# Kernel optimization log

Hardware: AMD Instinct MI355X
Metric: run time of the kernel (lower is better)

Reference implementation:

```python
import jax, jax.numpy as jnp
import numpy as np

B, QL, KL = 8, 2048, 2048
QD, KD, ED = 1024, 1024, 1024


def setup_inputs() -> dict:
    key = jax.random.key(0)
    ks = jax.random.split(key, 11)
    s = 0.02
    return {
        "query": jax.random.normal(ks[0], (B, QL, QD), jnp.float32),
        "key_value": jax.random.normal(ks[1], (B, KL, KD), jnp.float32),
        "mask": jnp.ones((B, QL, KL), jnp.int32),
        "Wq": jax.random.normal(ks[2], (QD, ED), jnp.float32) * s,
        "bq": jnp.zeros((ED,), jnp.float32),
        "Wk": jax.random.normal(ks[3], (KD, ED), jnp.float32) * s,
        "bk": jnp.zeros((ED,), jnp.float32),
        "Wv": jax.random.normal(ks[4], (KD, ED), jnp.float32) * s,
        "bv": jnp.zeros((ED,), jnp.float32),
        "Wo": jax.random.normal(ks[5], (ED, ED), jnp.float32) * s,
        "bo": jnp.zeros((ED,), jnp.float32),
    }


def reference(query, key_value, mask, Wq, bq, Wk, bk, Wv, bv, Wo, bo):
    # Linear projections
    Q = jnp.einsum('bqd,de->bqe', query, Wq) + bq      # (B, QL, E)
    K = jnp.einsum('bkd,de->bke', key_value, Wk) + bk  # (B, KL, E)
    V = jnp.einsum('bkd,de->bke', key_value, Wv) + bv  # (B, KL, E)
    scale = 1.0 / jnp.sqrt(jnp.asarray(Q.shape[-1], Q.dtype))
    scores = jnp.einsum('bqe,bke->bqk', Q, K) * scale  # (B, QL, KL)
    scores = jnp.where(mask == 0, -jnp.inf, scores)
    attn = jax.nn.softmax(scores, axis=-1)             # (B, QL, KL)
    # dropout is identity in eval mode
    attended = jnp.einsum('bqk,bke->bqe', attn, V)     # (B, QL, E)
    out = jnp.einsum('bqe,ef->bqf', attended, Wo) + bo
    return out, attn
```

## Files before the change

kernel.cpp:

```cpp
#include <hip/hip_runtime.h>
#include <hip/hip_bf16.h>
#include <math.h>


typedef __attribute__((ext_vector_type(8))) short short8;
typedef __attribute__((ext_vector_type(4))) float floatx4;

__device__ __forceinline__ unsigned short f2bf(float x) {
  return __builtin_bit_cast(unsigned short, __float2bfloat16(x));
}
__device__ __forceinline__ float bf2f(unsigned short s) {
  unsigned int u = ((unsigned int)s) << 16;
  return __builtin_bit_cast(float, u);
}

typedef const unsigned int __attribute__((address_space(1))) ga_u32;
typedef unsigned int __attribute__((address_space(3))) lds_u32;
__device__ __forceinline__ void gl_lds16(const void* g, void* l) {
  __builtin_amdgcn_global_load_lds((ga_u32*)g, (lds_u32*)l, 16, 0, 0);
}

template <int EPI>
__global__ __launch_bounds__(512, 2) void gemm8(
    const unsigned short* __restrict__ Ah,
    const unsigned short* __restrict__ Bh, void* __restrict__ Cp,
    unsigned short* __restrict__ Cl, const float* __restrict__ bias,
    float alpha, int M, int N, int K, int Mt, long long sA, long long sB,
    long long sC) {
  extern __shared__ char smem[];

  const int gx = gridDim.x;
  const int gxy = gx * gridDim.y;
  const int nwg = gxy * gridDim.z;
  const int orig = blockIdx.z * gxy + blockIdx.y * gx + blockIdx.x;
  const int wg = (orig & 7) * (nwg >> 3) + (orig >> 3);
  const int zb_i = wg / gxy;
  const int rem = wg - zb_i * gxy;
  const int by = rem / gx;
  const int bx = rem - by * gx;
  const int m0 = by * 256, n0 = bx * 256;
  const long long zb = zb_i;

  const unsigned short* Ag = Ah + zb * sA;
  const unsigned short* Bg = Bh + zb * sB;

  const int t = threadIdx.x;
  const int srow = t >> 3;
  const int skw = ((t & 7) << 3) ^ ((srow & 7) << 3);
  const unsigned short* aS = Ag + (long long)(m0 + srow) * K + skw;
  const unsigned short* bS = Bg + (long long)(n0 + srow) * K + skw;
  char* dstA = smem + t * 16;
  char* dstB = smem + 65536 + t * 16;

  const int lane = t & 63;
  const int wv = t >> 6, wy = wv >> 2, wx = wv & 3;
  const int lm = lane & 15, q = lane >> 4;
  const int x0 = (q << 4) ^ ((lm & 7) << 4);
  const int aB0 = (wy * 128 + lm) * 128;
  const int bB0 = 65536 + (wx * 64 + lm) * 128;
  const int aRd0 = aB0 + x0, aRd1 = aB0 + (x0 ^ 64);
  const int bRd0 = bB0 + x0, bRd1 = bB0 + (x0 ^ 64);

  floatx4 acc[8][4];
#pragma unroll
  for (int i = 0; i < 8; ++i)
#pragma unroll
    for (int j = 0; j < 4; ++j) acc[i][j] = (floatx4)(0.0f);

  short8 fa[4][2];
  short8 fb[2][2][2];

#pragma unroll
  for (int c = 0; c < 4; ++c) {
    gl_lds16(aS + (long long)(c * 64) * K, dstA + c * 8192);
    gl_lds16(bS + (long long)(c * 64) * K, dstB + c * 8192);
  }
  gl_lds16(aS + 64, dstA + 32768);
  gl_lds16(bS + 64, dstB + 32768);
  gl_lds16(aS + 64LL * K + 64, dstA + 32768 + 8192);
  gl_lds16(bS + 64LL * K + 64, dstB + 32768 + 8192);
  asm volatile("s_waitcnt vmcnt(4)" ::: "memory");
  __builtin_amdgcn_s_barrier();

  auto tile = [&](int kt, int bo, int nbo) {
    const bool p1 = (kt + 64) < K;
    const bool p2 = (kt + 128) < K;
#pragma unroll
    for (int mt = 0; mt < 4; ++mt) {
      fa[mt][0] = *(const short8*)(smem + (bo + aRd0 + mt * 2048));
      fa[mt][1] = *(const short8*)(smem + (bo + aRd1 + mt * 2048));
    }
#pragma unroll
    for (int nt = 0; nt < 2; ++nt) {
      fb[0][nt][0] = *(const short8*)(smem + (bo + bRd0 + nt * 2048));
      fb[0][nt][1] = *(const short8*)(smem + (bo + bRd1 + nt * 2048));
    }
    if (p1) {
      gl_lds16(aS + 128LL * K + (kt + 64), dstA + nbo + 16384);
      gl_lds16(bS + 128LL * K + (kt + 64), dstB + nbo + 16384);
    }
    __builtin_amdgcn_s_barrier();
    __builtin_amdgcn_s_setprio(1);
#pragma unroll
    for (int mt = 0; mt < 4; ++mt)
#pragma unroll
      for (int nt = 0; nt < 2; ++nt) {
        acc[mt][nt] = __builtin_amdgcn_mfma_f32_16x16x32_bf16(
            fa[mt][0], fb[0][nt][0], acc[mt][nt], 0, 0, 0);
        acc[mt][nt] = __builtin_amdgcn_mfma_f32_16x16x32_bf16(
            fa[mt][1], fb[0][nt][1], acc[mt][nt], 0, 0, 0);
      }
    __builtin_amdgcn_s_setprio(0);
    __builtin_amdgcn_s_barrier();
#pragma unroll
    for (int nt = 0; nt < 2; ++nt) {
      fb[1][nt][0] = *(const short8*)(smem + (bo + bRd0 + 4096 + nt * 2048));
      fb[1][nt][1] = *(const short8*)(smem + (bo + bRd1 + 4096 + nt * 2048));
    }
    if (p1) {
      gl_lds16(aS + 192LL * K + (kt + 64), dstA + nbo + 24576);
      gl_lds16(bS + 192LL * K + (kt + 64), dstB + nbo + 24576);
    }
    __builtin_amdgcn_s_barrier();
    __builtin_amdgcn_s_setprio(1);
#pragma unroll
    for (int mt = 0; mt < 4; ++mt)
#pragma unroll
      for (int nt = 0; nt < 2; ++nt) {
        acc[mt][2 + nt] = __builtin_amdgcn_mfma_f32_16x16x32_bf16(
            fa[mt][0], fb[1][nt][0], acc[mt][2 + nt], 0, 0, 0);
        acc[mt][2 + nt] = __builtin_amdgcn_mfma_f32_16x16x32_bf16(
            fa[mt][1], fb[1][nt][1], acc[mt][2 + nt], 0, 0, 0);
      }
    __builtin_amdgcn_s_setprio(0);
    __builtin_amdgcn_s_barrier();
#pragma unroll
    for (int mt = 0; mt < 4; ++mt) {
      fa[mt][0] = *(const short8*)(smem + (bo + aRd0 + 8192 + mt * 2048));
      fa[mt][1] = *(const short8*)(smem + (bo + aRd1 + 8192 + mt * 2048));
    }
    if (p2) {
      gl_lds16(aS + (kt + 128), dstA + bo);
      gl_lds16(bS + (kt + 128), dstB + bo);
    }
    __builtin_amdgcn_s_barrier();
    __builtin_amdgcn_s_setprio(1);
#pragma unroll
    for (int mt = 0; mt < 4; ++mt)
#pragma unroll
      for (int nt = 0; nt < 2; ++nt) {
        acc[4 + mt][nt] = __builtin_amdgcn_mfma_f32_16x16x32_bf16(
            fa[mt][0], fb[0][nt][0], acc[4 + mt][nt], 0, 0, 0);
        acc[4 + mt][nt] = __builtin_amdgcn_mfma_f32_16x16x32_bf16(
            fa[mt][1], fb[0][nt][1], acc[4 + mt][nt], 0, 0, 0);
      }
    __builtin_amdgcn_s_setprio(0);
    __builtin_amdgcn_s_barrier();
    if (p2) {
      gl_lds16(aS + 64LL * K + (kt + 128), dstA + bo + 8192);
      gl_lds16(bS + 64LL * K + (kt + 128), dstB + bo + 8192);
    }
    __builtin_amdgcn_s_barrier();
    __builtin_amdgcn_s_setprio(1);
#pragma unroll
    for (int mt = 0; mt < 4; ++mt)
#pragma unroll
      for (int nt = 0; nt < 2; ++nt) {
        acc[4 + mt][2 + nt] = __builtin_amdgcn_mfma_f32_16x16x32_bf16(
            fa[mt][0], fb[1][nt][0], acc[4 + mt][2 + nt], 0, 0, 0);
        acc[4 + mt][2 + nt] = __builtin_amdgcn_mfma_f32_16x16x32_bf16(
            fa[mt][1], fb[1][nt][1], acc[4 + mt][2 + nt], 0, 0, 0);
      }
    __builtin_amdgcn_s_setprio(0);
    if (p2) {
      asm volatile("s_waitcnt vmcnt(4)" ::: "memory");
    } else {
      asm volatile("s_waitcnt vmcnt(0)" ::: "memory");
    }
    __builtin_amdgcn_s_barrier();
  };

  for (int kt = 0; kt < K; kt += 128) {
    tile(kt, 0, 32768);
    tile(kt + 64, 32768, 0);
  }

#pragma unroll
  for (int ni = 0; ni < 4; ++ni) {
    const int col = n0 + wx * 64 + ni * 16 + lm;
    const float bvv = bias ? bias[col] : 0.0f;
#pragma unroll
    for (int mi = 0; mi < 8; ++mi) {
      const int rbase = m0 + wy * 128 + mi * 16 + q * 4;
      if constexpr (EPI == 3) {
        const int b = rbase / Mt;
        const int kk = rbase - b * Mt;
        unsigned short* dd =
            (unsigned short*)Cp + (long long)b * sC + (long long)col * Mt + kk;
        ushort4 pk;
        pk.x = f2bf(acc[mi][ni][0] * alpha + bvv);
        pk.y = f2bf(acc[mi][ni][1] * alpha + bvv);
        pk.z = f2bf(acc[mi][ni][2] * alpha + bvv);
        pk.w = f2bf(acc[mi][ni][3] * alpha + bvv);
        *reinterpret_cast<ushort4*>(dd) = pk;
      } else {
#pragma unroll
        for (int i = 0; i < 4; ++i) {
          const long long idx = zb * sC + (long long)(rbase + i) * N + col;
          const float x = acc[mi][ni][i] * alpha + bvv;
          if constexpr (EPI == 1) {
            ((unsigned short*)Cp)[idx] = f2bf(x);
          } else {
            const unsigned short h = f2bf(x);
            ((unsigned short*)Cp)[idx] = h;
            Cl[idx] = f2bf(x - bf2f(h));
          }
        }
      }
    }
  }
}

#define BM 128
#define BN 128
#define BK 32

template <int AMODE, bool BSPL, int EPI>
__global__ __launch_bounds__(256) void gemm_nt(
    const void* __restrict__ Apv, const unsigned short* __restrict__ Alp,
    const unsigned short* __restrict__ Bhp,
    const unsigned short* __restrict__ Blp, void* __restrict__ Cp,
    unsigned short* __restrict__ Cl, const float* __restrict__ bias,
    float alpha, int M, int N, int K, int Mt, long long sA, long long sB,
    long long sC) {
  __shared__ unsigned short As_h[BM * BK];
  __shared__ unsigned short Bs_h[BN * BK];
  __shared__ unsigned short As_l[(AMODE == 2) ? BM * BK : 8];
  __shared__ unsigned short Bs_l[BSPL ? BN * BK : 8];

  const int t = threadIdx.x;
  const int lane = t & 63;
  const int wave = t >> 6;
  const int wy = wave >> 1, wx = wave & 1;
  const int lm = lane & 15, q = lane >> 4;
  const int m0 = blockIdx.y * BM, n0 = blockIdx.x * BN;
  const long long zb = blockIdx.z;

  const unsigned short* Ahg = (const unsigned short*)Apv + zb * sA;
  const unsigned short* Alg = (AMODE == 2) ? (Alp + zb * sA) : nullptr;
  const unsigned short* Bhg = Bhp + zb * sB;
  const unsigned short* Blg = BSPL ? (Blp + zb * sB) : nullptr;

  floatx4 acc[4][4];
#pragma unroll
  for (int i = 0; i < 4; ++i)
#pragma unroll
    for (int j = 0; j < 4; ++j) acc[i][j] = (floatx4)(0.0f);

  const int ch_row = lane >> 2;
  const int ch_off = (lane & 3) << 3;

  for (int k0 = 0; k0 < K; k0 += BK) {
    __syncthreads();
#pragma unroll
    for (int j = 0; j < 2; ++j) {
      const int chunk = wave * 2 + j;
      const int row = chunk * 16 + ch_row;
      gl_lds16(Ahg + (long long)(m0 + row) * K + k0 + ch_off,
               &As_h[chunk * 512 + lane * 8]);
      if constexpr (AMODE == 2)
        gl_lds16(Alg + (long long)(m0 + row) * K + k0 + ch_off,
                 &As_l[chunk * 512 + lane * 8]);
    }
#pragma unroll
    for (int j = 0; j < 2; ++j) {
      const int chunk = wave * 2 + j;
      const int row = chunk * 16 + ch_row;
      gl_lds16(Bhg + (long long)(n0 + row) * K + k0 + ch_off,
               &Bs_h[chunk * 512 + lane * 8]);
      if constexpr (BSPL)
        gl_lds16(Blg + (long long)(n0 + row) * K + k0 + ch_off,
                 &Bs_l[chunk * 512 + lane * 8]);
    }
    __syncthreads();

    short8 fa[4], fb[4], fal[4], fbl[4];
#pragma unroll
    for (int mt = 0; mt < 4; ++mt) {
      const int row = wy * 64 + mt * 16 + lm;
      fa[mt] = *reinterpret_cast<const short8*>(&As_h[row * BK + q * 8]);
      if constexpr (AMODE == 2)
        fal[mt] = *reinterpret_cast<const short8*>(&As_l[row * BK + q * 8]);
    }
#pragma unroll
    for (int nt = 0; nt < 4; ++nt) {
      const int row = wx * 64 + nt * 16 + lm;
      fb[nt] = *reinterpret_cast<const short8*>(&Bs_h[row * BK + q * 8]);
      if constexpr (BSPL)
        fbl[nt] = *reinterpret_cast<const short8*>(&Bs_l[row * BK + q * 8]);
    }

#pragma unroll
    for (int mt = 0; mt < 4; ++mt)
#pragma unroll
      for (int nt = 0; nt < 4; ++nt) {
        acc[mt][nt] = __builtin_amdgcn_mfma_f32_16x16x32_bf16(
            fa[mt], fb[nt], acc[mt][nt], 0, 0, 0);
        if constexpr (AMODE == 2 && BSPL) {
          acc[mt][nt] = __builtin_amdgcn_mfma_f32_16x16x32_bf16(
              fa[mt], fbl[nt], acc[mt][nt], 0, 0, 0);
          acc[mt][nt] = __builtin_amdgcn_mfma_f32_16x16x32_bf16(
              fal[mt], fb[nt], acc[mt][nt], 0, 0, 0);
        }
      }
  }

#pragma unroll
  for (int nt = 0; nt < 4; ++nt) {
    const int col = n0 + wx * 64 + nt * 16 + lm;
    const float bv = bias ? bias[col] : 0.0f;
#pragma unroll
    for (int mt = 0; mt < 4; ++mt) {
      const int rbase = m0 + wy * 64 + mt * 16 + q * 4;
#pragma unroll
      for (int i = 0; i < 4; ++i) {
        const long long idx = zb * sC + (long long)(rbase + i) * N + col;
        const float x = acc[mt][nt][i] * alpha + bv;
        if constexpr (EPI == 0) {
          ((float*)Cp)[idx] = x;
        } else {
          ((unsigned short*)Cp)[idx] = f2bf(x);
        }
      }
    }
  }
}

__global__ __launch_bounds__(256) void cvt_bf16(const float* __restrict__ in,
                                                unsigned short* __restrict__ o,
                                                int n8) {
  const int i = blockIdx.x * 256 + threadIdx.x;
  if (i >= n8) return;
  const float4* p = reinterpret_cast<const float4*>(in) + (long long)i * 2;
  const float4 a = p[0], b = p[1];
  short8 h;
  h[0] = (short)f2bf(a.x); h[1] = (short)f2bf(a.y);
  h[2] = (short)f2bf(a.z); h[3] = (short)f2bf(a.w);
  h[4] = (short)f2bf(b.x); h[5] = (short)f2bf(b.y);
  h[6] = (short)f2bf(b.z); h[7] = (short)f2bf(b.w);
  reinterpret_cast<short8*>(o)[i] = h;
}

__global__ __launch_bounds__(256) void prep_w(const float* __restrict__ W,
                                              unsigned short* __restrict__ Th,
                                              unsigned short* __restrict__ Tl,
                                              int R, int C) {
  __shared__ float tile[32][33];
  const int c0 = blockIdx.x * 32, r0 = blockIdx.y * 32;
  const int tx = threadIdx.x & 31, ty = threadIdx.x >> 5;
#pragma unroll
  for (int i = 0; i < 4; ++i)
    tile[ty + i * 8][tx] = W[(long long)(r0 + ty + i * 8) * C + c0 + tx];
  __syncthreads();
#pragma unroll
  for (int i = 0; i < 4; ++i) {
    const float x = tile[tx][ty + i * 8];
    const long long idx = (long long)(c0 + ty + i * 8) * R + r0 + tx;
    const unsigned short h = f2bf(x);
    Th[idx] = h;
    if (Tl) Tl[idx] = f2bf(x - bf2f(h));
  }
}

__device__ __forceinline__ float wave_max64(float v) {
#pragma unroll
  for (int o = 32; o > 0; o >>= 1) v = fmaxf(v, __shfl_xor(v, o, 64));
  return v;
}
__device__ __forceinline__ float wave_sum64(float v) {
#pragma unroll
  for (int o = 32; o > 0; o >>= 1) v += __shfl_xor(v, o, 64);
  return v;
}

__global__ __launch_bounds__(256) void softmax_kernel(
    const unsigned short* __restrict__ Sh, const int* __restrict__ mask,
    float* __restrict__ attn, unsigned short* __restrict__ Ph) {
  const long long base = (long long)blockIdx.x * 2048;
  const int t = threadIdx.x;

  float vals[8];
  float lmax = -INFINITY;
#pragma unroll
  for (int g = 0; g < 2; ++g) {
    const int idx = (t + g * 256) * 4;
    const uint2 u = *reinterpret_cast<const uint2*>(Sh + base + idx);
    const int4 m = *reinterpret_cast<const int4*>(mask + base + idx);
    vals[g * 4 + 0] = m.x ? bf2f((unsigned short)(u.x & 0xffff)) : -INFINITY;
    vals[g * 4 + 1] = m.y ? bf2f((unsigned short)(u.x >> 16)) : -INFINITY;
    vals[g * 4 + 2] = m.z ? bf2f((unsigned short)(u.y & 0xffff)) : -INFINITY;
    vals[g * 4 + 3] = m.w ? bf2f((unsigned short)(u.y >> 16)) : -INFINITY;
  }
#pragma unroll
  for (int i = 0; i < 8; ++i) lmax = fmaxf(lmax, vals[i]);

  __shared__ float red[4];
  const float wm = wave_max64(lmax);
  if ((t & 63) == 0) red[t >> 6] = wm;
  __syncthreads();
  const float rmax = fmaxf(fmaxf(red[0], red[1]), fmaxf(red[2], red[3]));
  __syncthreads();

  float lsum = 0.0f;
#pragma unroll
  for (int i = 0; i < 8; ++i) {
    const float e = __expf(vals[i] - rmax);
    vals[i] = e;
    lsum += e;
  }
  const float wsum = wave_sum64(lsum);
  if ((t & 63) == 0) red[t >> 6] = wsum;
  __syncthreads();
  const float inv = 1.0f / (red[0] + red[1] + red[2] + red[3]);

#pragma unroll
  for (int g = 0; g < 2; ++g) {
    const int idx = (t + g * 256) * 4;
    float4 o;
    o.x = vals[g * 4 + 0] * inv;
    o.y = vals[g * 4 + 1] * inv;
    o.z = vals[g * 4 + 2] * inv;
    o.w = vals[g * 4 + 3] * inv;
    *reinterpret_cast<float4*>(attn + base + idx) = o;
    uint2 p;
    p.x = (unsigned)f2bf(o.x) | ((unsigned)f2bf(o.y) << 16);
    p.y = (unsigned)f2bf(o.z) | ((unsigned)f2bf(o.w) << 16);
    *reinterpret_cast<uint2*>(Ph + base + idx) = p;
  }
}

extern "C" void kernel_launch(void* const* d_in, const int* in_sizes, int n_in,
                              void* d_out, int out_size, void* d_ws,
                              size_t ws_size, hipStream_t stream) {
  const float* query = (const float*)d_in[0];
  const float* keyv = (const float*)d_in[1];
  const int* mask = (const int*)d_in[2];
  const float* Wq = (const float*)d_in[3];
  const float* bq = (const float*)d_in[4];
  const float* Wk = (const float*)d_in[5];
  const float* bk = (const float*)d_in[6];
  const float* Wv = (const float*)d_in[7];
  const float* bv = (const float*)d_in[8];
  const float* Wo = (const float*)d_in[9];
  const float* bo = (const float*)d_in[10];

  const int B = 8, QL = 2048, KL = 2048, D = 1024;
  const long long ML = (long long)B * QL;

  static int inited = 0;
  if (!inited) {
    hipFuncSetAttribute(reinterpret_cast<const void*>(&gemm8<1>),
                        hipFuncAttributeMaxDynamicSharedMemorySize, 131072);
    hipFuncSetAttribute(reinterpret_cast<const void*>(&gemm8<3>),
                        hipFuncAttributeMaxDynamicSharedMemorySize, 131072);
    hipFuncSetAttribute(reinterpret_cast<const void*>(&gemm8<4>),
                        hipFuncAttributeMaxDynamicSharedMemorySize, 131072);
    inited = 1;
  }

  float* out = (float*)d_out;
  float* attn = out + ML * D;

  char* w = (char*)d_ws;
  unsigned short* Qh = (unsigned short*)(w);
  unsigned short* Kh = (unsigned short*)(w + (32ll << 20));
  unsigned short* VTh = (unsigned short*)(w + (64ll << 20));
  unsigned short* Qf = (unsigned short*)(w + (96ll << 20));
  unsigned short* KVf = (unsigned short*)(w + (128ll << 20));
  unsigned short* Sh = (unsigned short*)(w + (96ll << 20));
  unsigned short* Ph = (unsigned short*)(w);
  unsigned short* Atth = (unsigned short*)(w + (96ll << 20));
  unsigned short* Attl = (unsigned short*)(w + (128ll << 20));
  unsigned short* WqT = (unsigned short*)(w + (160ll << 20));
  unsigned short* WkT = WqT + (1ll << 20);
  unsigned short* WvT = WkT + (1ll << 20);
  unsigned short* WoTh = WvT + (1ll << 20);
  unsigned short* WoTl = WoTh + (1ll << 20);

  const dim3 blk(256);
  const int n8 = (int)(ML * D / 8);

  cvt_bf16<<<dim3(n8 / 256), blk, 0, stream>>>(query, Qf, n8);
  cvt_bf16<<<dim3(n8 / 256), blk, 0, stream>>>(keyv, KVf, n8);

  prep_w<<<dim3(32, 32), blk, 0, stream>>>(Wq, WqT, nullptr, D, D);
  prep_w<<<dim3(32, 32), blk, 0, stream>>>(Wk, WkT, nullptr, D, D);
  prep_w<<<dim3(32, 32), blk, 0, stream>>>(Wv, WvT, nullptr, D, D);
  prep_w<<<dim3(32, 32), blk, 0, stream>>>(Wo, WoTh, WoTl, D, D);

  gemm8<1><<<dim3(D / 256, ML / 256, 1), 512, 131072, stream>>>(
      Qf, WqT, Qh, nullptr, bq, 1.0f, (int)ML, D, D, 1, 0, 0, 0);
  gemm8<1><<<dim3(D / 256, ML / 256, 1), 512, 131072, stream>>>(
      KVf, WkT, Kh, nullptr, bk, 1.0f, (int)ML, D, D, 1, 0, 0, 0);
  gemm8<3><<<dim3(D / 256, ML / 256, 1), 512, 131072, stream>>>(
      KVf, WvT, VTh, nullptr, bv, 1.0f, (int)ML, D, D, KL, 0, 0,
      (long long)D * KL);

  gemm8<1><<<dim3(KL / 256, QL / 256, B), 512, 131072, stream>>>(
      Qh, Kh, Sh, nullptr, nullptr, 0.03125f, QL, KL, D, 1,
      (long long)QL * D, (long long)KL * D, (long long)QL * KL);

  softmax_kernel<<<dim3((int)ML), blk, 0, stream>>>(Sh, mask, attn, Ph);

  gemm8<4><<<dim3(D / 256, QL / 256, B), 512, 131072, stream>>>(
      Ph, VTh, Atth, Attl, nullptr, 1.0f, QL, D, KL, 1, (long long)QL * KL,
      (long long)D * KL, (long long)QL * D);

  gemm_nt<2, true, 0><<<dim3(D / BN, (int)ML / BM, 1), blk, 0, stream>>>(
      Atth, Attl, WoTh, WoTl, out, nullptr, bo, 1.0f, (int)ML, D, D, 1, 0, 0,
      0);
}
```

Measured before the change: 825.8 us.

## Fold output projection into value projection by precomputing Wv·Wo

Uses associativity to compute V·Wo up front (KV times a precomputed Wv·Wo, plus bv·Wo as bias), so the attention PV GEMM writes the final fp32 output directly with bo added. This removes the separate split-precision output-projection GEMM and the hi/lo intermediate attended buffers. It adds a small 1024³ weight GEMM and a bias reduction, and reduces precision since the fused weight and V' are rounded to bf16.

New measurement: 728.1 us. 11.8% less time.

```diff
diff --git a/kernel.cpp b/kernel.cpp
--- a/kernel.cpp
+++ b/kernel.cpp
@@ -24,9 +24,8 @@
 __global__ __launch_bounds__(512, 2) void gemm8(
     const unsigned short* __restrict__ Ah,
     const unsigned short* __restrict__ Bh, void* __restrict__ Cp,
-    unsigned short* __restrict__ Cl, const float* __restrict__ bias,
-    float alpha, int M, int N, int K, int Mt, long long sA, long long sB,
-    long long sC) {
+    const float* __restrict__ bias, float alpha, int M, int N, int K, int Mt,
+    long long sA, long long sB, long long sC) {
   extern __shared__ char smem[];
 
   const int gx = gridDim.x;
@@ -208,128 +207,11 @@
         for (int i = 0; i < 4; ++i) {
           const long long idx = zb * sC + (long long)(rbase + i) * N + col;
           const float x = acc[mi][ni][i] * alpha + bvv;
-          if constexpr (EPI == 1) {
+          if constexpr (EPI == 0) {
+            ((float*)Cp)[idx] = x;
+          } else {
             ((unsigned short*)Cp)[idx] = f2bf(x);
-          } else {
-            const unsigned short h = f2bf(x);
-            ((unsigned short*)Cp)[idx] = h;
-            Cl[idx] = f2bf(x - bf2f(h));
           }
-        }
-      }
-    }
-  }
-}
-
-#define BM 128
-#define BN 128
-#define BK 32
-
-template <int AMODE, bool BSPL, int EPI>
-__global__ __launch_bounds__(256) void gemm_nt(
-    const void* __restrict__ Apv, const unsigned short* __restrict__ Alp,
-    const unsigned short* __restrict__ Bhp,
-    const unsigned short* __restrict__ Blp, void* __restrict__ Cp,
-    unsigned short* __restrict__ Cl, const float* __restrict__ bias,
-    float alpha, int M, int N, int K, int Mt, long long sA, long long sB,
-    long long sC) {
-  __shared__ unsigned short As_h[BM * BK];
-  __shared__ unsigned short Bs_h[BN * BK];
-  __shared__ unsigned short As_l[(AMODE == 2) ? BM * BK : 8];
-  __shared__ unsigned short Bs_l[BSPL ? BN * BK : 8];
-
-  const int t = threadIdx.x;
-  const int lane = t & 63;
-  const int wave = t >> 6;
-  const int wy = wave >> 1, wx = wave & 1;
-  const int lm = lane & 15, q = lane >> 4;
-  const int m0 = blockIdx.y * BM, n0 = blockIdx.x * BN;
-  const long long zb = blockIdx.z;
-
-  const unsigned short* Ahg = (const unsigned short*)Apv + zb * sA;
-  const unsigned short* Alg = (AMODE == 2) ? (Alp + zb * sA) : nullptr;
-  const unsigned short* Bhg = Bhp + zb * sB;
-  const unsigned short* Blg = BSPL ? (Blp + zb * sB) : nullptr;
-
-  floatx4 acc[4][4];
-#pragma unroll
-  for (int i = 0; i < 4; ++i)
-#pragma unroll
-    for (int j = 0; j < 4; ++j) acc[i][j] = (floatx4)(0.0f);
-
-  const int ch_row = lane >> 2;
-  const int ch_off = (lane & 3) << 3;
-
-  for (int k0 = 0; k0 < K; k0 += BK) {
-    __syncthreads();
-#pragma unroll
-    for (int j = 0; j < 2; ++j) {
-      const int chunk = wave * 2 + j;
-      const int row = chunk * 16 + ch_row;
-      gl_lds16(Ahg + (long long)(m0 + row) * K + k0 + ch_off,
-               &As_h[chunk * 512 + lane * 8]);
-      if constexpr (AMODE == 2)
-        gl_lds16(Alg + (long long)(m0 + row) * K + k0 + ch_off,
-                 &As_l[chunk * 512 + lane * 8]);
-    }
-#pragma unroll
-    for (int j = 0; j < 2; ++j) {
-      const int chunk = wave * 2 + j;
-      const int row = chunk * 16 + ch_row;
-      gl_lds16(Bhg + (long long)(n0 + row) * K + k0 + ch_off,
-               &Bs_h[chunk * 512 + lane * 8]);
-      if constexpr (BSPL)
-        gl_lds16(Blg + (long long)(n0 + row) * K + k0 + ch_off,
-                 &Bs_l[chunk * 512 + lane * 8]);
-    }
-    __syncthreads();
-
-    short8 fa[4], fb[4], fal[4], fbl[4];
-#pragma unroll
-    for (int mt = 0; mt < 4; ++mt) {
-      const int row = wy * 64 + mt * 16 + lm;
-      fa[mt] = *reinterpret_cast<const short8*>(&As_h[row * BK + q * 8]);
-      if constexpr (AMODE == 2)
-        fal[mt] = *reinterpret_cast<const short8*>(&As_l[row * BK + q * 8]);
-    }
-#pragma unroll
-    for (int nt = 0; nt < 4; ++nt) {
-      const int row = wx * 64 + nt * 16 + lm;
-      fb[nt] = *reinterpret_cast<const short8*>(&Bs_h[row * BK + q * 8]);
-      if constexpr (BSPL)
-        fbl[nt] = *reinterpret_cast<const short8*>(&Bs_l[row * BK + q * 8]);
-    }
-
-#pragma unroll
-    for (int mt = 0; mt < 4; ++mt)
-#pragma unroll
-      for (int nt = 0; nt < 4; ++nt) {
-        acc[mt][nt] = __builtin_amdgcn_mfma_f32_16x16x32_bf16(
-            fa[mt], fb[nt], acc[mt][nt], 0, 0, 0);
-        if constexpr (AMODE == 2 && BSPL) {
-          acc[mt][nt] = __builtin_amdgcn_mfma_f32_16x16x32_bf16(
-              fa[mt], fbl[nt], acc[mt][nt], 0, 0, 0);
-          acc[mt][nt] = __builtin_amdgcn_mfma_f32_16x16x32_bf16(
-              fal[mt], fb[nt], acc[mt][nt], 0, 0, 0);
-        }
-      }
-  }
-
-#pragma unroll
-  for (int nt = 0; nt < 4; ++nt) {
-    const int col = n0 + wx * 64 + nt * 16 + lm;
-    const float bv = bias ? bias[col] : 0.0f;
-#pragma unroll
-    for (int mt = 0; mt < 4; ++mt) {
-      const int rbase = m0 + wy * 64 + mt * 16 + q * 4;
-#pragma unroll
-      for (int i = 0; i < 4; ++i) {
-        const long long idx = zb * sC + (long long)(rbase + i) * N + col;
-        const float x = acc[mt][nt][i] * alpha + bv;
-        if constexpr (EPI == 0) {
-          ((float*)Cp)[idx] = x;
-        } else {
-          ((unsigned short*)Cp)[idx] = f2bf(x);
         }
       }
     }
@@ -353,7 +235,6 @@
 
 __global__ __launch_bounds__(256) void prep_w(const float* __restrict__ W,
                                               unsigned short* __restrict__ Th,
-                                              unsigned short* __restrict__ Tl,
                                               int R, int C) {
   __shared__ float tile[32][33];
   const int c0 = blockIdx.x * 32, r0 = blockIdx.y * 32;
@@ -366,10 +247,23 @@
   for (int i = 0; i < 4; ++i) {
     const float x = tile[tx][ty + i * 8];
     const long long idx = (long long)(c0 + ty + i * 8) * R + r0 + tx;
-    const unsigned short h = f2bf(x);
-    Th[idx] = h;
-    if (Tl) Tl[idx] = f2bf(x - bf2f(h));
-  }
+    Th[idx] = f2bf(x);
+  }
+}
+
+__global__ __launch_bounds__(256) void bias_wo(const float* __restrict__ bv,
+                                               const float* __restrict__ Wo,
+                                               float* __restrict__ bvWo) {
+  __shared__ float red[4][64];
+  const int fl = threadIdx.x & 63, eg = threadIdx.x >> 6;
+  const int f = blockIdx.x * 64 + fl;
+  float s = 0.0f;
+  const int e0 = eg * 256;
+  for (int e = e0; e < e0 + 256; ++e)
+    s += bv[e] * Wo[(long long)e * 1024 + f];
+  red[eg][fl] = s;
+  __syncthreads();
+  if (eg == 0) bvWo[f] = red[0][fl] + red[1][fl] + red[2][fl] + red[3][fl];
 }
 
 __device__ __forceinline__ float wave_max64(float v) {
@@ -459,12 +353,12 @@
 
   static int inited = 0;
   if (!inited) {
+    hipFuncSetAttribute(reinterpret_cast<const void*>(&gemm8<0>),
+                        hipFuncAttributeMaxDynamicSharedMemorySize, 131072);
     hipFuncSetAttribute(reinterpret_cast<const void*>(&gemm8<1>),
                         hipFuncAttributeMaxDynamicSharedMemorySize, 131072);
     hipFuncSetAttribute(reinterpret_cast<const void*>(&gemm8<3>),
                         hipFuncAttributeMaxDynamicSharedMemorySize, 131072);
-    hipFuncSetAttribute(reinterpret_cast<const void*>(&gemm8<4>),
-                        hipFuncAttributeMaxDynamicSharedMemorySize, 131072);
     inited = 1;
   }
 
@@ -474,49 +368,50 @@
   char* w = (char*)d_ws;
   unsigned short* Qh = (unsigned short*)(w);
   unsigned short* Kh = (unsigned short*)(w + (32ll << 20));
-  unsigned short* VTh = (unsigned short*)(w + (64ll << 20));
+  unsigned short* KVf = (unsigned short*)(w + (64ll << 20));
   unsigned short* Qf = (unsigned short*)(w + (96ll << 20));
-  unsigned short* KVf = (unsigned short*)(w + (128ll << 20));
-  unsigned short* Sh = (unsigned short*)(w + (96ll << 20));
+  unsigned short* VWoT = (unsigned short*)(w + (128ll << 20));
+  unsigned short* Sh = (unsigned short*)(w + (64ll << 20));
   unsigned short* Ph = (unsigned short*)(w);
-  unsigned short* Atth = (unsigned short*)(w + (96ll << 20));
-  unsigned short* Attl = (unsigned short*)(w + (128ll << 20));
   unsigned short* WqT = (unsigned short*)(w + (160ll << 20));
   unsigned short* WkT = WqT + (1ll << 20);
-  unsigned short* WvT = WkT + (1ll << 20);
-  unsigned short* WoTh = WvT + (1ll << 20);
-  unsigned short* WoTl = WoTh + (1ll << 20);
+  unsigned short* WoTh = WkT + (1ll << 20);
+  unsigned short* W2T = WoTh + (1ll << 20);
+  unsigned short* WvH = W2T + (1ll << 20);
+  float* bvWo = attn;
 
   const dim3 blk(256);
   const int n8 = (int)(ML * D / 8);
 
   cvt_bf16<<<dim3(n8 / 256), blk, 0, stream>>>(query, Qf, n8);
   cvt_bf16<<<dim3(n8 / 256), blk, 0, stream>>>(keyv, KVf, n8);
-
-  prep_w<<<dim3(32, 32), blk, 0, stream>>>(Wq, WqT, nullptr, D, D);
-  prep_w<<<dim3(32, 32), blk, 0, stream>>>(Wk, WkT, nullptr, D, D);
-  prep_w<<<dim3(32, 32), blk, 0, stream>>>(Wv, WvT, nullptr, D, D);
-  prep_w<<<dim3(32, 32), blk, 0, stream>>>(Wo, WoTh, WoTl, D, D);
+  cvt_bf16<<<dim3(512), blk, 0, stream>>>(Wv, WvH, D * D / 8);
+
+  prep_w<<<dim3(32, 32), blk, 0, stream>>>(Wq, WqT, D, D);
+  prep_w<<<dim3(32, 32), blk, 0, stream>>>(Wk, WkT, D, D);
+  prep_w<<<dim3(32, 32), blk, 0, stream>>>(Wo, WoTh, D, D);
+
+  bias_wo<<<dim3(16), blk, 0, stream>>>(bv, Wo, bvWo);
+
+  gemm8<1><<<dim3(D / 256, D / 256, 1), 512, 131072, stream>>>(
+      WoTh, WvH, W2T, nullptr, 1.0f, D, D, D, 1, 0, 0, 0);
 
   gemm8<1><<<dim3(D / 256, ML / 256, 1), 512, 131072, stream>>>(
-      Qf, WqT, Qh, nullptr, bq, 1.0f, (int)ML, D, D, 1, 0, 0, 0);
+      Qf, WqT, Qh, bq, 1.0f, (int)ML, D, D, 1, 0, 0, 0);
   gemm8<1><<<dim3(D / 256, ML / 256, 1), 512, 131072, stream>>>(
-      KVf, WkT, Kh, nullptr, bk, 1.0f, (int)ML, D, D, 1, 0, 0, 0);
+      KVf, WkT, Kh, bk, 1.0f, (int)ML, D, D, 1, 0, 0, 0);
+
   gemm8<3><<<dim3(D / 256, ML / 256, 1), 512, 131072, stream>>>(
-      KVf, WvT, VTh, nullptr, bv, 1.0f, (int)ML, D, D, KL, 0, 0,
+      KVf, W2T, VWoT, bvWo, 1.0f, (int)ML, D, D, KL, 0, 0,
       (long long)D * KL);
 
   gemm8<1><<<dim3(KL / 256, QL / 256, B), 512, 131072, stream>>>(
-      Qh, Kh, Sh, nullptr, nullptr, 0.03125f, QL, KL, D, 1,
+      Qh, Kh, Sh, nullptr, 0.03125f, QL, KL, D, 1,
       (long long)QL * D, (long long)KL * D, (long long)QL * KL);
 
   softmax_kernel<<<dim3((int)ML), blk, 0, stream>>>(Sh, mask, attn, Ph);
 
-  gemm8<4><<<dim3(D / 256, QL / 256, B), 512, 131072, stream>>>(
-      Ph, VTh, Atth, Attl, nullptr, 1.0f, QL, D, KL, 1, (long long)QL * KL,
+  gemm8<0><<<dim3(D / 256, QL / 256, B), 512, 131072, stream>>>(
+      Ph, VWoT, out, bo, 1.0f, QL, D, KL, 1, (long long)QL * KL,
       (long long)D * KL, (long long)QL * D);
-
-  gemm_nt<2, true, 0><<<dim3(D / BN, (int)ML / BM, 1), blk, 0, stream>>>(
-      Atth, Attl, WoTh, WoTl, out, nullptr, bo, 1.0f, (int)ML, D, D, 1, 0, 0,
-      0);
-}
+}
```
